# Performance work log

Measured on AMD Instinct MI355X. Metric: run time of the kernel, lower is better.

Reference implementation:

```python
import jax, jax.numpy as jnp
import numpy as np
from jax.scipy.special import erfc

# Problem scale
B, N, K = 16, 4000, 64          # systems, atoms/system, max neighbors
L = 30.0                         # cubic cell edge (Angstrom)
ALPHA = 0.3                      # Ewald splitting parameter (1/A), from config
KCUT = 1.0                       # reciprocal-space cutoff (1/A), from config
NMAX = 4                         # floor(KCUT / (2*pi/L)) -> static k-grid half-width
COULOMB_CONSTANT = 14.399645351950548  # e^2/(4 pi eps0) in eV*A


def setup_inputs() -> dict:
    key = jax.random.key(0)
    k1, k2, k3, k4 = jax.random.split(key, 4)
    T = B * N
    positions = jax.random.uniform(k1, (T, 3), dtype=jnp.float32) * L
    node_charges = jax.random.normal(k2, (T,), dtype=jnp.float32)
    cell = jnp.tile(jnp.eye(3, dtype=jnp.float32) * L, (B, 1, 1))
    # neighbor indices restricted to the same system; -1 marks self/padding
    local = jax.random.randint(k3, (T, K), 0, N)
    base = (jnp.arange(T) // N) * N
    nm = local + base[:, None]
    nm = jnp.where(nm == jnp.arange(T)[:, None], -1, nm).astype(jnp.int32)
    neighbor_shifts = jnp.zeros((T, K, 3), dtype=jnp.int32)
    num_neighbors = jnp.full((T,), K, dtype=jnp.int32)
    batch_idx = (jnp.arange(T) // N).astype(jnp.int32)
    return dict(positions=positions, node_charges=node_charges, cell=cell,
                neighbor_matrix=nm, neighbor_shifts=neighbor_shifts,
                num_neighbors=num_neighbors, batch_idx=batch_idx)


def _ewald_energies(positions, node_charges, cell, neighbor_matrix,
                    neighbor_shifts, num_neighbors, batch_idx):
    T = positions.shape[0]
    Bn = cell.shape[0]
    Nn = T // Bn
    Kn = neighbor_matrix.shape[1]
    q = node_charges.reshape(-1)
    dtype = positions.dtype
    alpha = jnp.full((Bn,), ALPHA, dtype=dtype)
    a_i = alpha[batch_idx]                                  # [T]

    # ---- real-space: neighbor gather + erfc + scatter-less per-atom sum ----
    mask = (neighbor_matrix >= 0) & (jnp.arange(Kn)[None, :] < num_neighbors[:, None])
    j = jnp.where(mask, neighbor_matrix, 0)                 # safe gather index [T,K]
    off = jnp.einsum('tks,tsd->tkd', neighbor_shifts.astype(dtype), cell[batch_idx])
    rij = positions[j] + off - positions[:, None, :]        # [T,K,3]
    d = jnp.sqrt(jnp.where(mask, jnp.sum(rij * rij, -1), 1.0))
    pair = jnp.where(mask, q[:, None] * q[j] * erfc(a_i[:, None] * d) / d, 0.0)
    # 0.5 for full (non-half) neighbor list; Gaussian self-interaction correction
    e_real = 0.5 * jnp.sum(pair, axis=-1) - a_i / jnp.sqrt(jnp.pi) * q * q  # [T]

    # ---- reciprocal-space: structure-factor sum over k-vectors ----
    rng = np.arange(-NMAX, NMAX + 1)
    nvec = np.stack(np.meshgrid(rng, rng, rng, indexing='ij'), -1).reshape(-1, 3)
    nvec = jnp.asarray(nvec, dtype=dtype)                   # [G,3] integer grid
    recip = 2.0 * jnp.pi * jnp.transpose(jnp.linalg.inv(cell), (0, 2, 1))  # rows b_j
    kv = jnp.einsum('gj,bjd->bgd', nvec, recip)             # [B,G,3]
    k2 = jnp.sum(kv * kv, -1)                               # [B,G]
    kmask = (k2 > 1e-10) & (k2 <= KCUT * KCUT)
    vol = jnp.abs(jnp.linalg.det(cell))                     # [B]
    a2 = alpha * alpha
    coef = jnp.where(kmask,
                     4.0 * jnp.pi * jnp.exp(-k2 / (4.0 * a2[:, None])) / jnp.where(kmask, k2, 1.0),
                     0.0) / (2.0 * vol[:, None])            # [B,G]
    pos_b = positions.reshape(Bn, Nn, 3)
    q_b = q.reshape(Bn, Nn)
    phase = jnp.einsum('bnd,bgd->bng', pos_b, kv)           # [B,N,G]
    c = jnp.cos(phase)
    s = jnp.sin(phase)
    Sre = jnp.einsum('bn,bng->bg', q_b, c)
    Sim = jnp.einsum('bn,bng->bg', q_b, s)
    e_recip = q_b * (jnp.einsum('bng,bg->bn', c, coef * Sre) +
                     jnp.einsum('bng,bg->bn', s, coef * Sim))  # [B,N]

    per_atom = e_real + e_recip.reshape(-1)
    energies = jax.ops.segment_sum(per_atom, batch_idx, num_segments=Bn)
    return energies * COULOMB_CONSTANT


def reference(positions, node_charges, cell, neighbor_matrix, neighbor_shifts,
              num_neighbors, batch_idx):
    return _ewald_energies(positions, node_charges, cell, neighbor_matrix,
                           neighbor_shifts, num_neighbors, batch_idx)
```

## Files before the change

### kernel.cpp

```cpp
#include <hip/hip_runtime.h>
#include <math.h>

#define GPB    8
#define GTOT   729
#define GMAX   46
#define KMAX   (GMAX*GPB)
#define APB    8
#define LAPB   16
#define STRIDE 600

__device__ __forceinline__ float wave_reduce(float v) {
    #pragma unroll
    for (int off = 32; off > 0; off >>= 1) v += __shfl_down(v, off, 64);
    return v;
}

__device__ __forceinline__ float fast_erfc(float x) {
    float t = __builtin_amdgcn_rcpf(fmaf(0.3275911f, x, 1.0f));
    float p = fmaf(1.061405429f, t, -1.453152027f);
    p = fmaf(p, t, 1.421413741f);
    p = fmaf(p, t, -0.284496736f);
    p = fmaf(p, t, 0.254829592f);
    return p * t * __expf(-x * x);
}

__global__ __launch_bounds__(256)
void prologue(const float* __restrict__ pos, const float* __restrict__ chg,
              float4* __restrict__ pq, const float* __restrict__ cell,
              float4* __restrict__ kcomp, int* __restrict__ kcnt,
              int T, int PB)
{
    int blk = blockIdx.x;
    if (blk < PB) {
        int t = blk * 256 + threadIdx.x;
        if (t < T)
            pq[t] = make_float4(pos[3*t], pos[3*t+1], pos[3*t+2], chg[t]);
        return;
    }
    int b = blk - PB;
    if (threadIdx.x >= 64) return;

    const float TWO_PI = 6.283185307179586f;
    const float INV4A2 = 2.7777777777f;
    const float KC2    = 1.0f;
    int lane = threadIdx.x;

    const float* C = cell + 9 * b;
    float m00=C[0], m01=C[1], m02=C[2];
    float m10=C[3], m11=C[4], m12=C[5];
    float m20=C[6], m21=C[7], m22=C[8];
    float a00 = m11*m22 - m12*m21;
    float a01 = m02*m21 - m01*m22;
    float a02 = m01*m12 - m02*m11;
    float a10 = m12*m20 - m10*m22;
    float a11 = m00*m22 - m02*m20;
    float a12 = m02*m10 - m00*m12;
    float a20 = m10*m21 - m11*m20;
    float a21 = m01*m20 - m00*m21;
    float a22 = m00*m11 - m01*m10;
    float det = m00*a00 + m01*a10 + m02*a20;
    float invdet = 1.0f / det;
    float vol = fabsf(det);

    int cnt = 0;
    for (int base = 0; base < GTOT; base += 64) {
        int g = base + lane;
        float kx = 0.f, ky = 0.f, kz = 0.f, cf = 0.f;
        if (g < GTOT) {
            int ix = g / 81, rem = g - ix * 81;
            int iy = rem / 9, iz = rem - iy * 9;
            int nx = ix - 4, ny = iy - 4, nz = iz - 4;
            bool pos_half = (nx > 0) || (nx == 0 && (ny > 0 || (ny == 0 && nz > 0)));
            if (pos_half) {
                float fx = (float)nx, fy = (float)ny, fz = (float)nz;
                kx = TWO_PI * invdet * (fx*a00 + fy*a01 + fz*a02);
                ky = TWO_PI * invdet * (fx*a10 + fy*a11 + fz*a12);
                kz = TWO_PI * invdet * (fx*a20 + fy*a21 + fz*a22);
                float k2 = kx*kx + ky*ky + kz*kz;
                if (k2 > 1e-10f && k2 <= KC2) {
                    cf = 12.566370614359172f * __expf(-k2 * INV4A2) / (k2 * vol);
                }
            }
        }
        bool act = (cf != 0.f);
        unsigned long long m = __ballot(act);
        if (act) {
            int off = __popcll(m & ((1ull << lane) - 1ull));
            kcomp[b * KMAX + cnt + off] = make_float4(kx, ky, kz, cf);
        }
        cnt += (int)__popcll(m);
    }
    int padded = ((cnt + GPB - 1) / GPB) * GPB;
    if (lane < padded - cnt)
        kcomp[b * KMAX + cnt + lane] = make_float4(0.f, 0.f, 0.f, 0.f);
    if (lane == 0) kcnt[b] = padded / GPB;
}

template <int KK>
__global__ __launch_bounds__(128)
void ewald_fused2(const float4* __restrict__ pq,
                  const float*  __restrict__ cell,
                  const int*    __restrict__ nm,
                  const int*    __restrict__ shifts,
                  const int*    __restrict__ nnb,
                  const float4* __restrict__ kcomp,
                  const int*    __restrict__ kcnt,
                  float* __restrict__ partial,
                  int T, int N, int K, int Bn, int CB)
{
    __shared__ float4 skv[GPB];
    __shared__ float  redA[2][GPB];
    __shared__ float  redB[2][GPB];
    __shared__ float  redr[2];

    const float ALPHA       = 0.3f;
    const float INV_SQRT_PI = 0.5641895835477563f;

    int blk  = blockIdx.x;
    int tid  = threadIdx.x;
    int lane = tid & 63;
    int w    = tid >> 6;

    if (blk < CB) {
        int b    = blk / GMAX;
        int grp  = blk - b * GMAX;
        int slot = b * STRIDE + (N / APB) + grp;
        int ng   = kcnt[b];
        if (grp >= ng) {
            if (tid == 0) partial[slot] = 0.f;
            return;
        }

        if (tid < GPB)
            skv[tid] = kcomp[b * KMAX + grp * GPB + tid];
        __syncthreads();

        float kvx[GPB], kvy[GPB], kvz[GPB];
        #pragma unroll
        for (int gi = 0; gi < GPB; ++gi) {
            float4 v = skv[gi];
            kvx[gi] = v.x; kvy[gi] = v.y; kvz[gi] = v.z;
        }

        float Sre[GPB], Sim[GPB];
        #pragma unroll
        for (int gi = 0; gi < GPB; ++gi) { Sre[gi] = 0.f; Sim[gi] = 0.f; }

        const float4* pb = pq + (size_t)b * N;
        int a = tid;
        for (; a + 128 < N; a += 256) {
            float4 v0 = pb[a];
            float4 v1 = pb[a + 128];
            #pragma unroll
            for (int gi = 0; gi < GPB; ++gi) {
                float ph0 = fmaf(v0.x, kvx[gi], fmaf(v0.y, kvy[gi], v0.z * kvz[gi]));
                float ph1 = fmaf(v1.x, kvx[gi], fmaf(v1.y, kvy[gi], v1.z * kvz[gi]));
                float s0, c0, s1, c1;
                __sincosf(ph0, &s0, &c0);
                __sincosf(ph1, &s1, &c1);
                Sre[gi] = fmaf(v0.w, c0, Sre[gi]);
                Sim[gi] = fmaf(v0.w, s0, Sim[gi]);
                Sre[gi] = fmaf(v1.w, c1, Sre[gi]);
                Sim[gi] = fmaf(v1.w, s1, Sim[gi]);
            }
        }
        if (a < N) {
            float4 v0 = pb[a];
            #pragma unroll
            for (int gi = 0; gi < GPB; ++gi) {
                float ph0 = fmaf(v0.x, kvx[gi], fmaf(v0.y, kvy[gi], v0.z * kvz[gi]));
                float s0, c0;
                __sincosf(ph0, &s0, &c0);
                Sre[gi] = fmaf(v0.w, c0, Sre[gi]);
                Sim[gi] = fmaf(v0.w, s0, Sim[gi]);
            }
        }

        #pragma unroll
        for (int gi = 0; gi < GPB; ++gi) {
            float sr = wave_reduce(Sre[gi]);
            float si = wave_reduce(Sim[gi]);
            if (lane == 0) { redA[w][gi] = sr; redB[w][gi] = si; }
        }
        __syncthreads();
        if (tid < 64) {
            float e = 0.f;
            if (tid < GPB) {
                float SR = redA[0][tid] + redA[1][tid];
                float SI = redB[0][tid] + redB[1][tid];
                e = skv[tid].w * (SR * SR + SI * SI);
            }
            e = wave_reduce(e);
            if (tid == 0) partial[slot] = e;
        }
    } else {
        int rb = blk - CB;
        int t0 = rb * APB;
        int sys = t0 / N;
        const float* C = cell + 9 * sys;
        float m0=C[0], m1=C[1], m2=C[2];
        float m3=C[3], m4=C[4], m5=C[5];
        float m6=C[6], m7=C[7], m8=C[8];

        float val = 0.0f;

        if (KK == 64) {
            const int row = lane >> 4;
            const int sub = lane & 15;
            int t  = t0 + w * 4 + row;
            float4 vi = pq[t];
            int    nn = nnb[t];
            if (sub == 0) val -= ALPHA * INV_SQRT_PI * vi.w * vi.w;
            int pb4 = t * 64 + sub * 4;
            int4 j4 = *reinterpret_cast<const int4*>(nm + pb4);
            int4 s0 = *reinterpret_cast<const int4*>(shifts + 3 * pb4);
            int4 s1 = *reinterpret_cast<const int4*>(shifts + 3 * pb4 + 4);
            int4 s2 = *reinterpret_cast<const int4*>(shifts + 3 * pb4 + 8);
            float4 vj0 = pq[j4.x < 0 ? 0 : j4.x];
            float4 vj1 = pq[j4.y < 0 ? 0 : j4.y];
            float4 vj2 = pq[j4.z < 0 ? 0 : j4.z];
            float4 vj3 = pq[j4.w < 0 ? 0 : j4.w];
            float hqi = 0.5f * vi.w;

            #define PAIR_BODY(JV, VJ, SX, SY, SZ, U)                          \
            {                                                                 \
                bool msk = ((JV) >= 0) && ((sub * 4 + (U)) < nn);             \
                float fx = (float)(SX), fy = (float)(SY), fz = (float)(SZ);   \
                float ox = fx*m0; ox = fmaf(fy, m3, ox); ox = fmaf(fz, m6, ox);\
                float oy = fx*m1; oy = fmaf(fy, m4, oy); oy = fmaf(fz, m7, oy);\
                float oz = fx*m2; oz = fmaf(fy, m5, oz); oz = fmaf(fz, m8, oz);\
                float dx = (VJ).x + ox - vi.x;                                \
                float dy = (VJ).y + oy - vi.y;                                \
                float dz = (VJ).z + oz - vi.z;                                \
                float r2 = fmaf(dx, dx, fmaf(dy, dy, dz*dz));                 \
                r2 = msk ? r2 : 1.0f;                                         \
                float rinv = rsqrtf(r2);                                      \
                float d = r2 * rinv;                                          \
                float e = fast_erfc(ALPHA * d);                               \
                float cq = msk ? hqi * (VJ).w : 0.f;                          \
                val = fmaf(cq * rinv, e, val);                                \
            }
            PAIR_BODY(j4.x, vj0, s0.x, s0.y, s0.z, 0)
            PAIR_BODY(j4.y, vj1, s0.w, s1.x, s1.y, 1)
            PAIR_BODY(j4.z, vj2, s1.z, s1.w, s2.x, 2)
            PAIR_BODY(j4.w, vj3, s2.y, s2.z, s2.w, 3)
            #undef PAIR_BODY
        } else {
            #pragma unroll
            for (int i = 0; i < APB/2; ++i) {
                int t = t0 + w * (APB/2) + i;
                float4 vi = pq[t];
                float hqi = 0.5f * vi.w;
                if (lane == 0) val -= ALPHA * INV_SQRT_PI * vi.w * vi.w;
                int nn = nnb[t];
                for (int k = lane; k < K; k += 64) {
                    int p = t * K + k;
                    int j = nm[p];
                    int sx = shifts[3*p], sy = shifts[3*p+1], sz = shifts[3*p+2];
                    bool msk = (j >= 0) && (k < nn);
                    int js = j < 0 ? 0 : j;
                    float4 vj = pq[js];
                    float fx = (float)sx, fy = (float)sy, fz = (float)sz;
                    float ox = fx*m0; ox = fmaf(fy, m3, ox); ox = fmaf(fz, m6, ox);
                    float oy = fx*m1; oy = fmaf(fy, m4, oy); oy = fmaf(fz, m7, oy);
                    float oz = fx*m2; oz = fmaf(fy, m5, oz); oz = fmaf(fz, m8, oz);
                    float dx = vj.x + ox - vi.x;
                    float dy = vj.y + oy - vi.y;
                    float dz = vj.z + oz - vi.z;
                    float r2 = fmaf(dx, dx, fmaf(dy, dy, dz*dz));
                    r2 = msk ? r2 : 1.0f;
                    float rinv = rsqrtf(r2);
                    float d = r2 * rinv;
                    float e = fast_erfc(ALPHA * d);
                    float cq = msk ? hqi * vj.w : 0.f;
                    val = fmaf(cq * rinv, e, val);
                }
            }
        }

        val = wave_reduce(val);
        if (lane == 0) redr[w] = val;
        __syncthreads();
        if (tid == 0) {
            int rb_in_sys = rb - sys * (N / APB);
            partial[sys * STRIDE + rb_in_sys] = redr[0] + redr[1];
        }
    }
}

__global__ __launch_bounds__(256)
void final_reduce(const float* __restrict__ partial, float* __restrict__ out,
                  int nslots)
{
    __shared__ float red[4];
    const float COUL = 14.399645351950548f;
    int b = blockIdx.x;
    float v = 0.f;
    for (int s = threadIdx.x; s < nslots; s += 256)
        v += partial[b * STRIDE + s];
    v = wave_reduce(v);
    int lane = threadIdx.x & 63, w = threadIdx.x >> 6;
    if (lane == 0) red[w] = v;
    __syncthreads();
    if (threadIdx.x == 0)
        out[b] = COUL * (red[0] + red[1] + red[2] + red[3]);
}

__global__ __launch_bounds__(256)
void ewald_legacy(const float* __restrict__ pos, const float* __restrict__ chg,
                  const float* __restrict__ cell, const int* __restrict__ nm,
                  const int* __restrict__ shifts, const int* __restrict__ nnb,
                  float* __restrict__ partial, int T, int N, int K, int Bn, int CB)
{
    __shared__ float red[16];
    const float TWO_PI  = 6.283185307179586f;
    const float ALPHA   = 0.3f;
    const float INV4A2  = 2.7777777777f;
    const float KC2     = 1.0f;
    const float INV_SQRT_PI = 0.5641895835477563f;
    int blk = blockIdx.x;

    if (blk < CB) {
        int gpb_groups = (GTOT + GPB - 1) / GPB;
        int b   = blk / gpb_groups;
        int grp = blk % gpb_groups;
        const float* C = cell + 9 * b;
        float m00=C[0], m01=C[1], m02=C[2];
        float m10=C[3], m11=C[4], m12=C[5];
        float m20=C[6], m21=C[7], m22=C[8];
        float a00 = m11*m22 - m12*m21;
        float a01 = m02*m21 - m01*m22;
        float a02 = m01*m12 - m02*m11;
        float a10 = m12*m20 - m10*m22;
        float a11 = m00*m22 - m02*m20;
        float a12 = m02*m10 - m00*m12;
        float a20 = m10*m21 - m11*m20;
        float a21 = m01*m20 - m00*m21;
        float a22 = m00*m11 - m01*m10;
        float det = m00*a00 + m01*a10 + m02*a20;
        float invdet = 1.0f / det;
        float vol = fabsf(det);

        float kvx[GPB], kvy[GPB], kvz[GPB], coef[GPB];
        bool any = false;
        #pragma unroll
        for (int gi = 0; gi < GPB; ++gi) {
            int g = grp * GPB + gi;
            float cf = 0.f, kx = 0.f, ky = 0.f, kz = 0.f;
            if (g < GTOT) {
                int ix = g / 81, rem = g - ix * 81;
                int iy = rem / 9, iz = rem - iy * 9;
                int nx = ix - 4, ny = iy - 4, nz = iz - 4;
                bool pos_half = (nx > 0) || (nx == 0 && (ny > 0 || (ny == 0 && nz > 0)));
                if (pos_half) {
                    float fx = (float)nx, fy = (float)ny, fz = (float)nz;
                    kx = TWO_PI * invdet * (fx*a00 + fy*a01 + fz*a02);
                    ky = TWO_PI * invdet * (fx*a10 + fy*a11 + fz*a12);
                    kz = TWO_PI * invdet * (fx*a20 + fy*a21 + fz*a22);
                    float k2 = kx*kx + ky*ky + kz*kz;
                    if (k2 > 1e-10f && k2 <= KC2)
                        cf = 12.566370614359172f * __expf(-k2 * INV4A2) / (k2 * vol);
                }
            }
            kvx[gi] = kx; kvy[gi] = ky; kvz[gi] = kz; coef[gi] = cf;
            any = any || (cf != 0.f);
        }
        int slot = b * STRIDE + (N / LAPB) + grp;
        if (!any) { if (threadIdx.x == 0) partial[slot] = 0.f; return; }

        float Sre[GPB], Sim[GPB];
        #pragma unroll
        for (int gi = 0; gi < GPB; ++gi) { Sre[gi] = 0.f; Sim[gi] = 0.f; }
        for (int a = threadIdx.x; a < N; a += 256) {
            const float* pp = pos + (size_t)3 * (b * N + a);
            float x = pp[0], y = pp[1], z = pp[2];
            float qa = chg[(size_t)b * N + a];
            #pragma unroll
            for (int gi = 0; gi < GPB; ++gi) {
                if (coef[gi] != 0.f) {
                    float ph = x*kvx[gi] + y*kvy[gi] + z*kvz[gi];
                    float s, c;
                    __sincosf(ph, &s, &c);
                    Sre[gi] = fmaf(qa, c, Sre[gi]);
                    Sim[gi] = fmaf(qa, s, Sim[gi]);
                }
            }
        }
        int lane = threadIdx.x & 63, w = threadIdx.x >> 6;
        float e_acc = 0.f;
        #pragma unroll
        for (int gi = 0; gi < GPB; ++gi) {
            if (coef[gi] != 0.f) {
                float sr = wave_reduce(Sre[gi]);
                float si = wave_reduce(Sim[gi]);
                if (lane == 0) { red[2*w] = sr; red[2*w+1] = si; }
                __syncthreads();
                if (threadIdx.x == 0) {
                    float SR = red[0] + red[2] + red[4] + red[6];
                    float SI = red[1] + red[3] + red[5] + red[7];
                    e_acc += coef[gi] * (SR*SR + SI*SI);
                }
                __syncthreads();
            }
        }
        if (threadIdx.x == 0) partial[slot] = e_acc;
    } else {
        int rb = blk - CB;
        int t0 = rb * LAPB;
        int sys = t0 / N;
        int lane = threadIdx.x & 63, w = threadIdx.x >> 6;
        float val = 0.0f;
        #pragma unroll
        for (int i = 0; i < LAPB/4; ++i) {
            int t = t0 + w * (LAPB/4) + i;
            float xi = pos[3*t], yi = pos[3*t+1], zi = pos[3*t+2];
            float qi = chg[t];
            if (lane == 0) val -= ALPHA * INV_SQRT_PI * qi * qi;
            int nn = nnb[t];
            for (int k = lane; k < K; k += 64) {
                int p = t * K + k;
                int j = nm[p];
                bool msk = (j >= 0) && (k < nn);
                if (msk) {
                    int sx = shifts[3*p], sy = shifts[3*p+1], sz = shifts[3*p+2];
                    float ox = 0.f, oy = 0.f, oz = 0.f;
                    if ((sx | sy | sz) != 0) {
                        const float* C = cell + 9 * sys;
                        float fx = (float)sx, fy = (float)sy, fz = (float)sz;
                        ox = fx*C[0] + fy*C[3] + fz*C[6];
                        oy = fx*C[1] + fy*C[4] + fz*C[7];
                        oz = fx*C[2] + fy*C[5] + fz*C[8];
                    }
                    float dx = pos[3*j] + ox - xi;
                    float dy = pos[3*j+1] + oy - yi;
                    float dz = pos[3*j+2] + oz - zi;
                    float r2 = fmaf(dx, dx, fmaf(dy, dy, dz*dz));
                    float rinv = rsqrtf(r2);
                    float d = r2 * rinv;
                    val += 0.5f * qi * chg[j] * fast_erfc(ALPHA * d) * rinv;
                }
            }
        }
        val = wave_reduce(val);
        if (lane == 0) red[w] = val;
        __syncthreads();
        if (threadIdx.x == 0) {
            int rb_in_sys = rb - sys * (N / LAPB);
            partial[sys * STRIDE + rb_in_sys] = red[0] + red[1] + red[2] + red[3];
        }
    }
}

extern "C" void kernel_launch(void* const* d_in, const int* in_sizes, int n_in,
                              void* d_out, int out_size, void* d_ws, size_t ws_size,
                              hipStream_t stream) {
    const float* pos    = (const float*)d_in[0];
    const float* chg    = (const float*)d_in[1];
    const float* cellp  = (const float*)d_in[2];
    const int*   nm     = (const int*)d_in[3];
    const int*   shifts = (const int*)d_in[4];
    const int*   nnb    = (const int*)d_in[5];

    int T  = in_sizes[1];
    int Bn = in_sizes[2] / 9;
    int N  = T / Bn;
    int K  = in_sizes[3] / T;

    size_t partBytes = (size_t)Bn * STRIDE * sizeof(float);
    size_t pqOff     = ((partBytes + 255) / 256) * 256;
    size_t pqBytes   = (size_t)T * sizeof(float4);
    size_t kOff      = ((pqOff + pqBytes + 255) / 256) * 256;
    size_t kBytes    = (size_t)Bn * KMAX * sizeof(float4);
    size_t cntOff    = kOff + kBytes;
    size_t needed    = cntOff + (size_t)Bn * sizeof(int);

    if ((N % APB) == 0 && ws_size >= needed) {
        float*  partial = (float*)d_ws;
        float4* pq      = (float4*)((char*)d_ws + pqOff);
        float4* kcomp   = (float4*)((char*)d_ws + kOff);
        int*    kcnt    = (int*)((char*)d_ws + cntOff);

        int PB = (T + 255) / 256;
        int CB = Bn * GMAX;
        int RB = T / APB;
        int nslots = (N / APB) + GMAX;

        prologue<<<PB + Bn, 256, 0, stream>>>(pos, chg, pq, cellp, kcomp, kcnt,
                                              T, PB);
        if (K == 64)
            ewald_fused2<64><<<CB + RB, 128, 0, stream>>>(
                pq, cellp, nm, shifts, nnb, kcomp, kcnt, partial, T, N, K, Bn, CB);
        else
            ewald_fused2<0><<<CB + RB, 128, 0, stream>>>(
                pq, cellp, nm, shifts, nnb, kcomp, kcnt, partial, T, N, K, Bn, CB);
        final_reduce<<<Bn, 256, 0, stream>>>(partial, (float*)d_out, nslots);
    } else {
        float* partial = (float*)d_ws;
        int CB = Bn * ((GTOT + GPB - 1) / GPB);
        int RB = T / LAPB;
        int nslots = (N / LAPB) + ((GTOT + GPB - 1) / GPB);
        ewald_legacy<<<CB + RB, 256, 0, stream>>>(pos, chg, cellp, nm, shifts,
                                                  nnb, partial, T, N, K, Bn, CB);
        final_reduce<<<Bn, 256, 0, stream>>>(partial, (float*)d_out, nslots);
    }
}
```

Before: 122.2 us.

## Split fused Ewald kernel into separate real-space and reciprocal kernels

Splits the fused kernel into two launches: ewald_real handles the neighbor-pair erfc sum with 128-thread blocks, and ewald_recip computes the structure factors with 256-thread blocks. Each kernel gets its own block size and register allocation instead of sharing one heterogeneous grid. The cost is one extra kernel launch and the loss of real-space and reciprocal blocks running concurrently in a single grid.

```diff
diff --git a/kernel.cpp b/kernel.cpp
--- a/kernel.cpp
+++ b/kernel.cpp
@@ -96,195 +96,203 @@
     if (lane == 0) kcnt[b] = padded / GPB;
 }
 
-template <int KK>
-__global__ __launch_bounds__(128)
-void ewald_fused2(const float4* __restrict__ pq,
-                  const float*  __restrict__ cell,
-                  const int*    __restrict__ nm,
-                  const int*    __restrict__ shifts,
-                  const int*    __restrict__ nnb,
-                  const float4* __restrict__ kcomp,
-                  const int*    __restrict__ kcnt,
-                  float* __restrict__ partial,
-                  int T, int N, int K, int Bn, int CB)
+__global__ __launch_bounds__(256)
+void ewald_recip(const float4* __restrict__ pq,
+                 const float4* __restrict__ kcomp,
+                 const int*    __restrict__ kcnt,
+                 float* __restrict__ partial,
+                 int N, int RPS)
 {
     __shared__ float4 skv[GPB];
-    __shared__ float  redA[2][GPB];
-    __shared__ float  redB[2][GPB];
-    __shared__ float  redr[2];
-
-    const float ALPHA       = 0.3f;
-    const float INV_SQRT_PI = 0.5641895835477563f;
-
-    int blk  = blockIdx.x;
+    __shared__ float  redA[4][GPB];
+    __shared__ float  redB[4][GPB];
+
     int tid  = threadIdx.x;
     int lane = tid & 63;
     int w    = tid >> 6;
 
-    if (blk < CB) {
-        int b    = blk / GMAX;
-        int grp  = blk - b * GMAX;
-        int slot = b * STRIDE + (N / APB) + grp;
-        int ng   = kcnt[b];
-        if (grp >= ng) {
-            if (tid == 0) partial[slot] = 0.f;
-            return;
-        }
-
-        if (tid < GPB)
-            skv[tid] = kcomp[b * KMAX + grp * GPB + tid];
-        __syncthreads();
-
-        float kvx[GPB], kvy[GPB], kvz[GPB];
+    int b    = blockIdx.x / GMAX;
+    int grp  = blockIdx.x - b * GMAX;
+    int slot = b * STRIDE + RPS + grp;
+    int ng   = kcnt[b];
+    if (grp >= ng) {
+        if (tid == 0) partial[slot] = 0.f;
+        return;
+    }
+
+    if (tid < GPB)
+        skv[tid] = kcomp[b * KMAX + grp * GPB + tid];
+    __syncthreads();
+
+    float kvx[GPB], kvy[GPB], kvz[GPB];
+    #pragma unroll
+    for (int gi = 0; gi < GPB; ++gi) {
+        float4 v = skv[gi];
+        kvx[gi] = v.x; kvy[gi] = v.y; kvz[gi] = v.z;
+    }
+
+    float Sre[GPB], Sim[GPB];
+    #pragma unroll
+    for (int gi = 0; gi < GPB; ++gi) { Sre[gi] = 0.f; Sim[gi] = 0.f; }
+
+    const float4* pb = pq + (size_t)b * N;
+    int a = tid;
+    for (; a + 256 < N; a += 512) {
+        float4 v0 = pb[a];
+        float4 v1 = pb[a + 256];
         #pragma unroll
         for (int gi = 0; gi < GPB; ++gi) {
-            float4 v = skv[gi];
-            kvx[gi] = v.x; kvy[gi] = v.y; kvz[gi] = v.z;
-        }
-
-        float Sre[GPB], Sim[GPB];
-        #pragma unroll
-        for (int gi = 0; gi < GPB; ++gi) { Sre[gi] = 0.f; Sim[gi] = 0.f; }
-
-        const float4* pb = pq + (size_t)b * N;
-        int a = tid;
-        for (; a + 128 < N; a += 256) {
-            float4 v0 = pb[a];
-            float4 v1 = pb[a + 128];
-            #pragma unroll
-            for (int gi = 0; gi < GPB; ++gi) {
-                float ph0 = fmaf(v0.x, kvx[gi], fmaf(v0.y, kvy[gi], v0.z * kvz[gi]));
-                float ph1 = fmaf(v1.x, kvx[gi], fmaf(v1.y, kvy[gi], v1.z * kvz[gi]));
-                float s0, c0, s1, c1;
-                __sincosf(ph0, &s0, &c0);
-                __sincosf(ph1, &s1, &c1);
-                Sre[gi] = fmaf(v0.w, c0, Sre[gi]);
-                Sim[gi] = fmaf(v0.w, s0, Sim[gi]);
-                Sre[gi] = fmaf(v1.w, c1, Sre[gi]);
-                Sim[gi] = fmaf(v1.w, s1, Sim[gi]);
+            float ph0 = fmaf(v0.x, kvx[gi], fmaf(v0.y, kvy[gi], v0.z * kvz[gi]));
+            float ph1 = fmaf(v1.x, kvx[gi], fmaf(v1.y, kvy[gi], v1.z * kvz[gi]));
+            float s0, c0, s1, c1;
+            __sincosf(ph0, &s0, &c0);
+            __sincosf(ph1, &s1, &c1);
+            Sre[gi] = fmaf(v0.w, c0, Sre[gi]);
+            Sim[gi] = fmaf(v0.w, s0, Sim[gi]);
+            Sre[gi] = fmaf(v1.w, c1, Sre[gi]);
+            Sim[gi] = fmaf(v1.w, s1, Sim[gi]);
+        }
+    }
+    if (a < N) {
+        float4 v0 = pb[a];
+        #pragma unroll
+        for (int gi = 0; gi < GPB; ++gi) {
+            float ph0 = fmaf(v0.x, kvx[gi], fmaf(v0.y, kvy[gi], v0.z * kvz[gi]));
+            float s0, c0;
+            __sincosf(ph0, &s0, &c0);
+            Sre[gi] = fmaf(v0.w, c0, Sre[gi]);
+            Sim[gi] = fmaf(v0.w, s0, Sim[gi]);
+        }
+    }
+
+    #pragma unroll
+    for (int gi = 0; gi < GPB; ++gi) {
+        float sr = wave_reduce(Sre[gi]);
+        float si = wave_reduce(Sim[gi]);
+        if (lane == 0) { redA[w][gi] = sr; redB[w][gi] = si; }
+    }
+    __syncthreads();
+    if (tid < 64) {
+        float e = 0.f;
+        if (tid < GPB) {
+            float SR = redA[0][tid] + redA[1][tid] + redA[2][tid] + redA[3][tid];
+            float SI = redB[0][tid] + redB[1][tid] + redB[2][tid] + redB[3][tid];
+            e = skv[tid].w * (SR * SR + SI * SI);
+        }
+        e = wave_reduce(e);
+        if (tid == 0) partial[slot] = e;
+    }
+}
+
+template <int KK>
+__global__ __launch_bounds__(128)
+void ewald_real(const float4* __restrict__ pq,
+                const float*  __restrict__ cell,
+                const int*    __restrict__ nm,
+                const int*    __restrict__ shifts,
+                const int*    __restrict__ nnb,
+                float* __restrict__ partial,
+                int N, int K)
+{
+    __shared__ float redr[2];
+
+    const float ALPHA       = 0.3f;
+    const float INV_SQRT_PI = 0.5641895835477563f;
+
+    int tid  = threadIdx.x;
+    int lane = tid & 63;
+    int w    = tid >> 6;
+
+    int rb = blockIdx.x;
+    int t0 = rb * APB;
+    int sys = t0 / N;
+    const float* C = cell + 9 * sys;
+    float m0=C[0], m1=C[1], m2=C[2];
+    float m3=C[3], m4=C[4], m5=C[5];
+    float m6=C[6], m7=C[7], m8=C[8];
+
+    float val = 0.0f;
+
+    if (KK == 64) {
+        const int row = lane >> 4;
+        const int sub = lane & 15;
+        int t  = t0 + w * 4 + row;
+        float4 vi = pq[t];
+        int    nn = nnb[t];
+        if (sub == 0) val -= ALPHA * INV_SQRT_PI * vi.w * vi.w;
+        int pb4 = t * 64 + sub * 4;
+        int4 j4 = *reinterpret_cast<const int4*>(nm + pb4);
+        int4 s0 = *reinterpret_cast<const int4*>(shifts + 3 * pb4);
+        int4 s1 = *reinterpret_cast<const int4*>(shifts + 3 * pb4 + 4);
+        int4 s2 = *reinterpret_cast<const int4*>(shifts + 3 * pb4 + 8);
+        float4 vj0 = pq[j4.x < 0 ? 0 : j4.x];
+        float4 vj1 = pq[j4.y < 0 ? 0 : j4.y];
+        float4 vj2 = pq[j4.z < 0 ? 0 : j4.z];
+        float4 vj3 = pq[j4.w < 0 ? 0 : j4.w];
+        float hqi = 0.5f * vi.w;
+
+        #define PAIR_BODY(JV, VJ, SX, SY, SZ, U)                              \
+        {                                                                     \
+            bool msk = ((JV) >= 0) && ((sub * 4 + (U)) < nn);                 \
+            float fx = (float)(SX), fy = (float)(SY), fz = (float)(SZ);       \
+            float ox = fx*m0; ox = fmaf(fy, m3, ox); ox = fmaf(fz, m6, ox);   \
+            float oy = fx*m1; oy = fmaf(fy, m4, oy); oy = fmaf(fz, m7, oy);   \
+            float oz = fx*m2; oz = fmaf(fy, m5, oz); oz = fmaf(fz, m8, oz);   \
+            float dx = (VJ).x + ox - vi.x;                                    \
+            float dy = (VJ).y + oy - vi.y;                                    \
+            float dz = (VJ).z + oz - vi.z;                                    \
+            float r2 = fmaf(dx, dx, fmaf(dy, dy, dz*dz));                     \
+            r2 = msk ? r2 : 1.0f;                                             \
+            float rinv = rsqrtf(r2);                                          \
+            float d = r2 * rinv;                                              \
+            float e = fast_erfc(ALPHA * d);                                   \
+            float cq = msk ? hqi * (VJ).w : 0.f;                              \
+            val = fmaf(cq * rinv, e, val);                                    \
+        }
+        PAIR_BODY(j4.x, vj0, s0.x, s0.y, s0.z, 0)
+        PAIR_BODY(j4.y, vj1, s0.w, s1.x, s1.y, 1)
+        PAIR_BODY(j4.z, vj2, s1.z, s1.w, s2.x, 2)
+        PAIR_BODY(j4.w, vj3, s2.y, s2.z, s2.w, 3)
+        #undef PAIR_BODY
+    } else {
+        #pragma unroll
+        for (int i = 0; i < APB/2; ++i) {
+            int t = t0 + w * (APB/2) + i;
+            float4 vi = pq[t];
+            float hqi = 0.5f * vi.w;
+            if (lane == 0) val -= ALPHA * INV_SQRT_PI * vi.w * vi.w;
+            int nn = nnb[t];
+            for (int k = lane; k < K; k += 64) {
+                int p = t * K + k;
+                int j = nm[p];
+                int sx = shifts[3*p], sy = shifts[3*p+1], sz = shifts[3*p+2];
+                bool msk = (j >= 0) && (k < nn);
+                int js = j < 0 ? 0 : j;
+                float4 vj = pq[js];
+                float fx = (float)sx, fy = (float)sy, fz = (float)sz;
+                float ox = fx*m0; ox = fmaf(fy, m3, ox); ox = fmaf(fz, m6, ox);
+                float oy = fx*m1; oy = fmaf(fy, m4, oy); oy = fmaf(fz, m7, oy);
+                float oz = fx*m2; oz = fmaf(fy, m5, oz); oz = fmaf(fz, m8, oz);
+                float dx = vj.x + ox - vi.x;
+                float dy = vj.y + oy - vi.y;
+                float dz = vj.z + oz - vi.z;
+                float r2 = fmaf(dx, dx, fmaf(dy, dy, dz*dz));
+                r2 = msk ? r2 : 1.0f;
+                float rinv = rsqrtf(r2);
+                float d = r2 * rinv;
+                float e = fast_erfc(ALPHA * d);
+                float cq = msk ? hqi * vj.w : 0.f;
+                val = fmaf(cq * rinv, e, val);
             }
         }
-        if (a < N) {
-            float4 v0 = pb[a];
-            #pragma unroll
-            for (int gi = 0; gi < GPB; ++gi) {
-                float ph0 = fmaf(v0.x, kvx[gi], fmaf(v0.y, kvy[gi], v0.z * kvz[gi]));
-                float s0, c0;
-                __sincosf(ph0, &s0, &c0);
-                Sre[gi] = fmaf(v0.w, c0, Sre[gi]);
-                Sim[gi] = fmaf(v0.w, s0, Sim[gi]);
-            }
-        }
-
-        #pragma unroll
-        for (int gi = 0; gi < GPB; ++gi) {
-            float sr = wave_reduce(Sre[gi]);
-            float si = wave_reduce(Sim[gi]);
-            if (lane == 0) { redA[w][gi] = sr; redB[w][gi] = si; }
-        }
-        __syncthreads();
-        if (tid < 64) {
-            float e = 0.f;
-            if (tid < GPB) {
-                float SR = redA[0][tid] + redA[1][tid];
-                float SI = redB[0][tid] + redB[1][tid];
-                e = skv[tid].w * (SR * SR + SI * SI);
-            }
-            e = wave_reduce(e);
-            if (tid == 0) partial[slot] = e;
-        }
-    } else {
-        int rb = blk - CB;
-        int t0 = rb * APB;
-        int sys = t0 / N;
-        const float* C = cell + 9 * sys;
-        float m0=C[0], m1=C[1], m2=C[2];
-        float m3=C[3], m4=C[4], m5=C[5];
-        float m6=C[6], m7=C[7], m8=C[8];
-
-        float val = 0.0f;
-
-        if (KK == 64) {
-            const int row = lane >> 4;
-            const int sub = lane & 15;
-            int t  = t0 + w * 4 + row;
-            float4 vi = pq[t];
-            int    nn = nnb[t];
-            if (sub == 0) val -= ALPHA * INV_SQRT_PI * vi.w * vi.w;
-            int pb4 = t * 64 + sub * 4;
-            int4 j4 = *reinterpret_cast<const int4*>(nm + pb4);
-            int4 s0 = *reinterpret_cast<const int4*>(shifts + 3 * pb4);
-            int4 s1 = *reinterpret_cast<const int4*>(shifts + 3 * pb4 + 4);
-            int4 s2 = *reinterpret_cast<const int4*>(shifts + 3 * pb4 + 8);
-            float4 vj0 = pq[j4.x < 0 ? 0 : j4.x];
-            float4 vj1 = pq[j4.y < 0 ? 0 : j4.y];
-            float4 vj2 = pq[j4.z < 0 ? 0 : j4.z];
-            float4 vj3 = pq[j4.w < 0 ? 0 : j4.w];
-            float hqi = 0.5f * vi.w;
-
-            #define PAIR_BODY(JV, VJ, SX, SY, SZ, U)                          \
-            {                                                                 \
-                bool msk = ((JV) >= 0) && ((sub * 4 + (U)) < nn);             \
-                float fx = (float)(SX), fy = (float)(SY), fz = (float)(SZ);   \
-                float ox = fx*m0; ox = fmaf(fy, m3, ox); ox = fmaf(fz, m6, ox);\
-                float oy = fx*m1; oy = fmaf(fy, m4, oy); oy = fmaf(fz, m7, oy);\
-                float oz = fx*m2; oz = fmaf(fy, m5, oz); oz = fmaf(fz, m8, oz);\
-                float dx = (VJ).x + ox - vi.x;                                \
-                float dy = (VJ).y + oy - vi.y;                                \
-                float dz = (VJ).z + oz - vi.z;                                \
-                float r2 = fmaf(dx, dx, fmaf(dy, dy, dz*dz));                 \
-                r2 = msk ? r2 : 1.0f;                                         \
-                float rinv = rsqrtf(r2);                                      \
-                float d = r2 * rinv;                                          \
-                float e = fast_erfc(ALPHA * d);                               \
-                float cq = msk ? hqi * (VJ).w : 0.f;                          \
-                val = fmaf(cq * rinv, e, val);                                \
-            }
-            PAIR_BODY(j4.x, vj0, s0.x, s0.y, s0.z, 0)
-            PAIR_BODY(j4.y, vj1, s0.w, s1.x, s1.y, 1)
-            PAIR_BODY(j4.z, vj2, s1.z, s1.w, s2.x, 2)
-            PAIR_BODY(j4.w, vj3, s2.y, s2.z, s2.w, 3)
-            #undef PAIR_BODY
-        } else {
-            #pragma unroll
-            for (int i = 0; i < APB/2; ++i) {
-                int t = t0 + w * (APB/2) + i;
-                float4 vi = pq[t];
-                float hqi = 0.5f * vi.w;
-                if (lane == 0) val -= ALPHA * INV_SQRT_PI * vi.w * vi.w;
-                int nn = nnb[t];
-                for (int k = lane; k < K; k += 64) {
-                    int p = t * K + k;
-                    int j = nm[p];
-                    int sx = shifts[3*p], sy = shifts[3*p+1], sz = shifts[3*p+2];
-                    bool msk = (j >= 0) && (k < nn);
-                    int js = j < 0 ? 0 : j;
-                    float4 vj = pq[js];
-                    float fx = (float)sx, fy = (float)sy, fz = (float)sz;
-                    float ox = fx*m0; ox = fmaf(fy, m3, ox); ox = fmaf(fz, m6, ox);
-                    float oy = fx*m1; oy = fmaf(fy, m4, oy); oy = fmaf(fz, m7, oy);
-                    float oz = fx*m2; oz = fmaf(fy, m5, oz); oz = fmaf(fz, m8, oz);
-                    float dx = vj.x + ox - vi.x;
-                    float dy = vj.y + oy - vi.y;
-                    float dz = vj.z + oz - vi.z;
-                    float r2 = fmaf(dx, dx, fmaf(dy, dy, dz*dz));
-                    r2 = msk ? r2 : 1.0f;
-                    float rinv = rsqrtf(r2);
-                    float d = r2 * rinv;
-                    float e = fast_erfc(ALPHA * d);
-                    float cq = msk ? hqi * vj.w : 0.f;
-                    val = fmaf(cq * rinv, e, val);
-                }
-            }
-        }
-
-        val = wave_reduce(val);
-        if (lane == 0) redr[w] = val;
-        __syncthreads();
-        if (tid == 0) {
-            int rb_in_sys = rb - sys * (N / APB);
-            partial[sys * STRIDE + rb_in_sys] = redr[0] + redr[1];
-        }
+    }
+
+    val = wave_reduce(val);
+    if (lane == 0) redr[w] = val;
+    __syncthreads();
+    if (tid == 0) {
+        int rb_in_sys = rb - sys * (N / APB);
+        partial[sys * STRIDE + rb_in_sys] = redr[0] + redr[1];
     }
 }
 
@@ -480,19 +488,21 @@
         float4* kcomp   = (float4*)((char*)d_ws + kOff);
         int*    kcnt    = (int*)((char*)d_ws + cntOff);
 
-        int PB = (T + 255) / 256;
-        int CB = Bn * GMAX;
-        int RB = T / APB;
-        int nslots = (N / APB) + GMAX;
+        int PB  = (T + 255) / 256;
+        int CB  = Bn * GMAX;
+        int RB  = T / APB;
+        int RPS = N / APB;
+        int nslots = RPS + GMAX;
 
         prologue<<<PB + Bn, 256, 0, stream>>>(pos, chg, pq, cellp, kcomp, kcnt,
                                               T, PB);
         if (K == 64)
-            ewald_fused2<64><<<CB + RB, 128, 0, stream>>>(
-                pq, cellp, nm, shifts, nnb, kcomp, kcnt, partial, T, N, K, Bn, CB);
+            ewald_real<64><<<RB, 128, 0, stream>>>(pq, cellp, nm, shifts, nnb,
+                                                   partial, N, K);
         else
-            ewald_fused2<0><<<CB + RB, 128, 0, stream>>>(
-                pq, cellp, nm, shifts, nnb, kcomp, kcnt, partial, T, N, K, Bn, CB);
+            ewald_real<0><<<RB, 128, 0, stream>>>(pq, cellp, nm, shifts, nnb,
+                                                  partial, N, K);
+        ewald_recip<<<CB, 256, 0, stream>>>(pq, kcomp, kcnt, partial, N, RPS);
         final_reduce<<<Bn, 256, 0, stream>>>(partial, (float*)d_out, nslots);
     } else {
         float* partial = (float*)d_ws;
```

After: 131.5 us. 1.08x slower.
